# Optimization experiments

Hardware: AMD Instinct MI355X
Metric: run time of the kernel (lower is better)

## Reference

```python
import jax, jax.numpy as jnp
import numpy as np

N_OBJ = 20000
N_TRI = 100000
D = 512      # input_dim_obj == input_dim_pred == output_dim
H = 512      # hidden_dim


def _kaiming(key, fan_out, fan_in):
    return jax.random.normal(key, (fan_out, fan_in), jnp.float32) * jnp.sqrt(2.0 / fan_in)


def setup_inputs() -> dict:
    key = jax.random.key(0)
    ks = jax.random.split(key, 12)
    obj_vecs = jax.random.normal(ks[0], (N_OBJ, D), jnp.float32)
    pred_vecs = jax.random.normal(ks[1], (N_TRI, D), jnp.float32)
    edges = jax.random.randint(ks[2], (N_TRI, 2), 0, N_OBJ, jnp.int32)
    Din1 = 2 * D + D            # net1 input: 1536
    Dout1 = 2 * H + D           # net1 output: 1536
    return {
        "obj_vecs": obj_vecs,
        "pred_vecs": pred_vecs,
        "edges": edges,
        "W1": _kaiming(ks[3], H, Din1), "b1": jnp.zeros((H,), jnp.float32),
        "W2": _kaiming(ks[4], Dout1, H), "b2": jnp.zeros((Dout1,), jnp.float32),
        "V1": _kaiming(ks[5], H, H), "c1": jnp.zeros((H,), jnp.float32),
        "V2": _kaiming(ks[6], D, H), "c2": jnp.zeros((D,), jnp.float32),
        "P_obj": jax.random.normal(ks[7], (D, D), jnp.float32) * (1.0 / jnp.sqrt(D)),
        "pb_obj": jnp.zeros((D,), jnp.float32),
        "P_pred": jax.random.normal(ks[8], (D, D), jnp.float32) * (1.0 / jnp.sqrt(D)),
        "pb_pred": jnp.zeros((D,), jnp.float32),
    }


def reference(obj_vecs, pred_vecs, edges, W1, b1, W2, b2, V1, c1, V2, c2,
              P_obj, pb_obj, P_pred, pb_pred):
    num_objs = obj_vecs.shape[0]
    s_idx = edges[:, 0]
    o_idx = edges[:, 1]
    # gather + concat: [T, 2*D + D]
    cur_t = jnp.concatenate([obj_vecs[s_idx], pred_vecs, obj_vecs[o_idx]], axis=1)
    # net1: Linear -> ReLU -> Linear -> ReLU (final_nonlinearity=True)
    h = jax.nn.relu(cur_t @ W1.T + b1)
    new_t = jax.nn.relu(h @ W2.T + b2)            # [T, 2H + D]
    new_s = new_t[:, :H]
    new_p = new_t[:, H:H + D]
    new_o = new_t[:, H + D:2 * H + D]
    # scatter_add pooling
    pooled = jax.ops.segment_sum(new_s, s_idx, num_segments=num_objs)
    pooled = pooled + jax.ops.segment_sum(new_o, o_idx, num_segments=num_objs)
    # avg pooling normalization
    ones = jnp.ones((edges.shape[0],), jnp.float32)
    counts = jax.ops.segment_sum(ones, s_idx, num_segments=num_objs)
    counts = counts + jax.ops.segment_sum(ones, o_idx, num_segments=num_objs)
    counts = jnp.maximum(counts, 1.0)
    pooled = pooled / counts[:, None]
    # net2: Linear -> ReLU -> Linear -> ReLU
    g = jax.nn.relu(pooled @ V1.T + c1)
    new_obj = jax.nn.relu(g @ V2.T + c2)
    # residual projections
    new_obj = new_obj + obj_vecs @ P_obj.T + pb_obj
    new_p = new_p + pred_vecs @ P_pred.T + pb_pred
    return new_obj, new_p
```

## Files before the change

kernel.cpp:

```cpp
#include <hip/hip_runtime.h>
#include <stdint.h>

#define NOBJ 20000
#define NTRI 100000

typedef unsigned short ushort_t;
typedef __attribute__((ext_vector_type(8))) short short8;
typedef __attribute__((ext_vector_type(4))) float float4v;

enum { MODE_H = 0, MODE_G = 2, MODE_OBJ = 3, MODE_PRED = 4, MODE_SO = 5, MODE_P = 6 };

__device__ __forceinline__ ushort_t f2bf(float f) {
    union { float f; unsigned int i; } x;
    x.f = f;
    unsigned int r = x.i + 0x7fffu + ((x.i >> 16) & 1u);
    return (ushort_t)(r >> 16);
}

__device__ __forceinline__ void gload_lds16(const ushort_t* g, short8* l) {
    __builtin_amdgcn_global_load_lds((const __attribute__((address_space(1))) void*)g,
                                     (__attribute__((address_space(3))) void*)l,
                                     16, 0, 0);
}

__global__ void __launch_bounds__(256) cvt_k(const float* __restrict__ src,
                                             ushort_t* __restrict__ dst, int n4) {
    int i = blockIdx.x * 256 + threadIdx.x;
    if (i >= n4) return;
    const float4* s4 = (const float4*)src;
    float4 v = s4[i];
    ushort_t o[4] = {f2bf(v.x), f2bf(v.y), f2bf(v.z), f2bf(v.w)};
    *(uint64_t*)(dst + 4 * (size_t)i) = *(const uint64_t*)o;
}

__global__ void __launch_bounds__(256) hist_k(const int* __restrict__ edges,
                                              int* __restrict__ counts_s,
                                              int* __restrict__ counts_o, int n2) {
    int i = blockIdx.x * 256 + threadIdx.x;
    if (i >= n2) return;
    int obj = edges[i];
    if (i & 1) atomicAdd(&counts_o[obj], 1);
    else       atomicAdd(&counts_s[obj], 1);
}

__global__ void __launch_bounds__(256) scan_k(const int* __restrict__ counts,
                                              int* __restrict__ offs,
                                              int* __restrict__ cur, int n) {
    __shared__ int lds[256];
    const int CHUNK = 80;
    int t = threadIdx.x;
    int base = t * CHUNK;
    int s = 0;
    for (int j = 0; j < CHUNK; ++j) {
        int i = base + j;
        if (i < n) s += counts[i];
    }
    lds[t] = s;
    __syncthreads();
    for (int off = 1; off < 256; off <<= 1) {
        int v = (t >= off) ? lds[t - off] : 0;
        __syncthreads();
        lds[t] += v;
        __syncthreads();
    }
    int run = lds[t] - s;
    for (int j = 0; j < CHUNK; ++j) {
        int i = base + j;
        if (i < n) {
            offs[i] = run;
            cur[i] = run;
            run += counts[i];
        } else if (i == n) {
            offs[n] = run;
        }
    }
}

__global__ void __launch_bounds__(256) fill_k(const int* __restrict__ edges,
                                              int* __restrict__ cur_s, int* __restrict__ cur_o,
                                              int* __restrict__ perm_s, int* __restrict__ perm_o,
                                              int n) {
    int t = blockIdx.x * 256 + threadIdx.x;
    if (t >= n) return;
    int s = edges[2 * t];
    int o = edges[2 * t + 1];
    perm_s[atomicAdd(&cur_s[s], 1)] = t;
    perm_o[atomicAdd(&cur_o[o], 1)] = t;
}

template <int PASS>
__global__ void __launch_bounds__(256)
pool_k(const ushort_t* __restrict__ nst, const int* __restrict__ offs_s,
       const int* __restrict__ offs_o, float* __restrict__ pooled) {
    int wave = threadIdx.x >> 6;
    int lane = threadIdx.x & 63;
    int obj = blockIdx.x * 4 + wave;
    if (obj >= NOBJ) return;
    const int* offs = (PASS == 0) ? offs_s : offs_o;
    int s = offs[obj], e = offs[obj + 1];
    float acc[8];
#pragma unroll
    for (int j = 0; j < 8; ++j) acc[j] = 0.f;
    for (int i = s; i < e; ++i) {
        uint4 v = *(const uint4*)(nst + (size_t)i * 512 + lane * 8);
        acc[0] += __uint_as_float(v.x << 16);
        acc[1] += __uint_as_float(v.x & 0xffff0000u);
        acc[2] += __uint_as_float(v.y << 16);
        acc[3] += __uint_as_float(v.y & 0xffff0000u);
        acc[4] += __uint_as_float(v.z << 16);
        acc[5] += __uint_as_float(v.z & 0xffff0000u);
        acc[6] += __uint_as_float(v.w << 16);
        acc[7] += __uint_as_float(v.w & 0xffff0000u);
    }
    float* prow = pooled + (size_t)obj * 512 + lane * 8;
    if (PASS == 0) {
        *(float4*)(prow)     = make_float4(acc[0], acc[1], acc[2], acc[3]);
        *(float4*)(prow + 4) = make_float4(acc[4], acc[5], acc[6], acc[7]);
    } else {
        float4 a0 = *(const float4*)(prow);
        float4 a1 = *(const float4*)(prow + 4);
        int deg = (offs_s[obj + 1] - offs_s[obj]) + (offs_o[obj + 1] - offs_o[obj]);
        float inv = 1.f / (float)((deg > 1) ? deg : 1);
        *(float4*)(prow)     = make_float4((acc[0] + a0.x) * inv, (acc[1] + a0.y) * inv,
                                           (acc[2] + a0.z) * inv, (acc[3] + a0.w) * inv);
        *(float4*)(prow + 4) = make_float4((acc[4] + a1.x) * inv, (acc[5] + a1.y) * inv,
                                           (acc[6] + a1.z) * inv, (acc[7] + a1.w) * inv);
    }
}

template <int MODE>
__global__ void __launch_bounds__(256)
gtc_gemm(const ushort_t* __restrict__ A, const ushort_t* __restrict__ Bw,
         const float* __restrict__ bias,
         const ushort_t* __restrict__ A2, const ushort_t* __restrict__ B2,
         const float* __restrict__ bias2,
         const int* __restrict__ idx,
         const ushort_t* __restrict__ objv, const ushort_t* __restrict__ predv,
         const float* __restrict__ addend,
         void* __restrict__ outv,
         int M, int K, int lda)
{
    __shared__ short8 sA[1024];
    __shared__ short8 sB[1024];
    __shared__ int sIdx[128];
    __shared__ int oIdx[128];

    const int tid  = threadIdx.x;
    const int lane = tid & 63;
    const int wave = tid >> 6;
    const int wm   = wave & 1;
    const int wn   = wave >> 1;
    const int quad = lane >> 4;
    const int lr   = lane & 15;
    const int m0   = blockIdx.y * 128;
    const int n0   = blockIdx.x * 128;

    if (MODE == MODE_H) {
        if (tid < 128) {
            int t = m0 + tid;
            if (t >= M) t = M - 1;
            sIdx[tid] = idx[2 * t];
            oIdx[tid] = idx[2 * t + 1];
        }
        __syncthreads();
    } else if (MODE == MODE_SO) {
        if (tid < 128) {
            int t = m0 + tid;
            if (t >= M) t = M - 1;
            sIdx[tid] = idx[t];
        }
        __syncthreads();
    }

    float4v acc[4][4];
#pragma unroll
    for (int i = 0; i < 4; ++i)
#pragma unroll
        for (int j = 0; j < 4; ++j)
            acc[i][j] = (float4v){0.f, 0.f, 0.f, 0.f};

    const int npass = (MODE == MODE_OBJ) ? 2 : 1;
    for (int pass = 0; pass < npass; ++pass) {
        const ushort_t* Ap = (pass == 0) ? A : A2;
        const ushort_t* Bp = (pass == 0) ? Bw : B2;

        for (int k0 = 0; k0 < K; k0 += 64) {
            __syncthreads();
#pragma unroll
            for (int i = 0; i < 4; ++i) {
                int g  = i * 256 + tid;
                int kg = g >> 7;
                int m  = g & 127;
                int krow = k0 + kg * 8;
                const ushort_t* src;
                if (MODE == MODE_H) {
                    int t = m0 + m;
                    if (t >= M) t = M - 1;
                    if (krow < 512)
                        src = objv + (size_t)sIdx[m] * 512 + krow;
                    else if (krow < 1024)
                        src = predv + (size_t)t * 512 + (krow - 512);
                    else
                        src = objv + (size_t)oIdx[m] * 512 + (krow - 1024);
                } else if (MODE == MODE_SO) {
                    src = Ap + (size_t)sIdx[m] * (size_t)K + krow;
                } else {
                    int r = m0 + m;
                    if (r >= M) r = M - 1;
                    src = Ap + (size_t)r * (size_t)lda + krow;
                }
                gload_lds16(src, &sA[g]);
            }
#pragma unroll
            for (int i = 0; i < 4; ++i) {
                int g  = i * 256 + tid;
                int kg = g >> 7;
                int n  = g & 127;
                gload_lds16(Bp + (size_t)(n0 + n) * K + k0 + kg * 8, &sB[g]);
            }
            __syncthreads();

#pragma unroll
            for (int kk = 0; kk < 2; ++kk) {
                short8 af[4], bfv[4];
#pragma unroll
                for (int t = 0; t < 4; ++t)
                    af[t] = sA[(kk * 4 + quad) * 128 + wm * 64 + t * 16 + lr];
#pragma unroll
                for (int t = 0; t < 4; ++t)
                    bfv[t] = sB[(kk * 4 + quad) * 128 + wn * 64 + t * 16 + lr];
#pragma unroll
                for (int ti = 0; ti < 4; ++ti)
#pragma unroll
                    for (int tj = 0; tj < 4; ++tj)
                        acc[ti][tj] = __builtin_amdgcn_mfma_f32_16x16x32_bf16(
                            af[ti], bfv[tj], acc[ti][tj], 0, 0, 0);
            }
        }

        if (MODE == MODE_OBJ && pass == 0) {
#pragma unroll
            for (int tj = 0; tj < 4; ++tj) {
                float b = bias[n0 + wn * 64 + tj * 16 + lr];
#pragma unroll
                for (int ti = 0; ti < 4; ++ti)
#pragma unroll
                    for (int r = 0; r < 4; ++r)
                        acc[ti][tj][r] = fmaxf(acc[ti][tj][r] + b, 0.f);
            }
        }
    }

    float bcol[4];
#pragma unroll
    for (int tj = 0; tj < 4; ++tj) {
        int col = n0 + wn * 64 + tj * 16 + lr;
        const float* bptr = (MODE == MODE_OBJ) ? bias2 : bias;
        bcol[tj] = bptr[col];
    }

#pragma unroll
    for (int ti = 0; ti < 4; ++ti) {
#pragma unroll
        for (int r = 0; r < 4; ++r) {
            int row = m0 + wm * 64 + ti * 16 + quad * 4 + r;
            if (row >= M) continue;
#pragma unroll
            for (int tj = 0; tj < 4; ++tj) {
                int col = n0 + wn * 64 + tj * 16 + lr;
                float v = acc[ti][tj][r];
                if (MODE == MODE_H || MODE == MODE_G || MODE == MODE_SO) {
                    v = fmaxf(v + bcol[tj], 0.f);
                    ((ushort_t*)outv)[(size_t)row * 512 + col] = f2bf(v);
                } else if (MODE == MODE_P) {
                    v = fmaxf(v + bcol[tj], 0.f) + addend[(size_t)row * 512 + col];
                    ((float*)outv)[(size_t)row * 512 + col] = v;
                } else if (MODE == MODE_OBJ) {
                    ((float*)outv)[(size_t)row * 512 + col] = v + bcol[tj];
                } else {
                    v = v + bcol[tj];
                    if (addend) v += addend[(size_t)row * 512 + col];
                    ((float*)outv)[(size_t)row * 512 + col] = v;
                }
            }
        }
    }
}

extern "C" void kernel_launch(void* const* d_in, const int* in_sizes, int n_in,
                              void* d_out, int out_size, void* d_ws, size_t ws_size,
                              hipStream_t stream) {
    const float* obj    = (const float*)d_in[0];
    const float* pred   = (const float*)d_in[1];
    const int*   edges  = (const int*)d_in[2];
    const float* W1     = (const float*)d_in[3];
    const float* b1     = (const float*)d_in[4];
    const float* W2     = (const float*)d_in[5];
    const float* b2     = (const float*)d_in[6];
    const float* V1     = (const float*)d_in[7];
    const float* c1     = (const float*)d_in[8];
    const float* V2     = (const float*)d_in[9];
    const float* c2     = (const float*)d_in[10];
    const float* Pobj   = (const float*)d_in[11];
    const float* pbobj  = (const float*)d_in[12];
    const float* Ppred  = (const float*)d_in[13];
    const float* pbpred = (const float*)d_in[14];

    char* ws = (char*)d_ws;
    ushort_t* h       = (ushort_t*)(ws + 0);
    ushort_t* bfPred  = (ushort_t*)(ws + 102400000);
    ushort_t* nst     = bfPred;
    ushort_t* bfObj   = (ushort_t*)(ws + 204800000);
    ushort_t* bfW1    = (ushort_t*)(ws + 225280000);
    char* csr = ws + 225280000;
    int* counts_s = (int*)(csr + 0);
    int* counts_o = (int*)(csr + 80000);
    int* offs_s   = (int*)(csr + 160000);
    int* offs_o   = (int*)(csr + 240064);
    int* cur_s    = (int*)(csr + 320128);
    int* cur_o    = (int*)(csr + 400128);
    int* perm_s   = (int*)(csr + 480128);
    int* perm_o   = (int*)(csr + 880128);
    ushort_t* bfW2    = (ushort_t*)(ws + 226852864);
    ushort_t* bfV1    = (ushort_t*)(ws + 228425728);
    ushort_t* bfV2    = (ushort_t*)(ws + 228950016);
    ushort_t* bfPobj  = (ushort_t*)(ws + 229474304);
    ushort_t* bfPpred = (ushort_t*)(ws + 229998592);
    ushort_t* pooledn = (ushort_t*)(ws + 0);
    ushort_t* gbuf    = (ushort_t*)(ws + 20480000);

    float* out_obj = (float*)d_out;
    float* out_p   = out_obj + (size_t)NOBJ * 512;
    float* pooled = out_obj;

    cvt_k<<<dim3(10000), dim3(256), 0, stream>>>(obj,   bfObj,   10240000 / 4);
    cvt_k<<<dim3(50000), dim3(256), 0, stream>>>(pred,  bfPred,  51200000 / 4);
    cvt_k<<<dim3(768),   dim3(256), 0, stream>>>(W1,    bfW1,    786432 / 4);
    cvt_k<<<dim3(768),   dim3(256), 0, stream>>>(W2,    bfW2,    786432 / 4);
    cvt_k<<<dim3(256),   dim3(256), 0, stream>>>(V1,    bfV1,    262144 / 4);
    cvt_k<<<dim3(256),   dim3(256), 0, stream>>>(V2,    bfV2,    262144 / 4);
    cvt_k<<<dim3(256),   dim3(256), 0, stream>>>(Pobj,  bfPobj,  262144 / 4);
    cvt_k<<<dim3(256),   dim3(256), 0, stream>>>(Ppred, bfPpred, 262144 / 4);

    gtc_gemm<MODE_PRED><<<dim3(4, 782), dim3(256), 0, stream>>>(
        bfPred, bfPpred, pbpred, nullptr, nullptr, nullptr,
        nullptr, nullptr, nullptr, nullptr, out_p, NTRI, 512, 512);

    gtc_gemm<MODE_H><<<dim3(4, 782), dim3(256), 0, stream>>>(
        nullptr, bfW1, b1, nullptr, nullptr, nullptr,
        edges, bfObj, bfPred, nullptr, h, NTRI, 1536, 1536);

    hipMemsetAsync(counts_s, 0, 160000, stream);
    hist_k<<<dim3(782), dim3(256), 0, stream>>>(edges, counts_s, counts_o, 2 * NTRI);
    scan_k<<<dim3(1), dim3(256), 0, stream>>>(counts_s, offs_s, cur_s, NOBJ);
    scan_k<<<dim3(1), dim3(256), 0, stream>>>(counts_o, offs_o, cur_o, NOBJ);
    fill_k<<<dim3(391), dim3(256), 0, stream>>>(edges, cur_s, cur_o, perm_s, perm_o, NTRI);

    gtc_gemm<MODE_SO><<<dim3(4, 782), dim3(256), 0, stream>>>(
        h, bfW2, b2, nullptr, nullptr, nullptr,
        perm_s, nullptr, nullptr, nullptr, nst, NTRI, 512, 512);
    pool_k<0><<<dim3(5000), dim3(256), 0, stream>>>(nst, offs_s, offs_o, pooled);

    gtc_gemm<MODE_SO><<<dim3(4, 782), dim3(256), 0, stream>>>(
        h, bfW2 + 1024 * 512, b2 + 1024, nullptr, nullptr, nullptr,
        perm_o, nullptr, nullptr, nullptr, nst, NTRI, 512, 512);
    pool_k<1><<<dim3(5000), dim3(256), 0, stream>>>(nst, offs_s, offs_o, pooled);

    gtc_gemm<MODE_P><<<dim3(4, 782), dim3(256), 0, stream>>>(
        h, bfW2 + 512 * 512, b2 + 512, nullptr, nullptr, nullptr,
        nullptr, nullptr, nullptr, out_p, out_p, NTRI, 512, 512);

    cvt_k<<<dim3(10000), dim3(256), 0, stream>>>(pooled, pooledn, 10240000 / 4);

    gtc_gemm<MODE_G><<<dim3(4, 157), dim3(256), 0, stream>>>(
        pooledn, bfV1, c1, nullptr, nullptr, nullptr,
        nullptr, nullptr, nullptr, nullptr, gbuf, NOBJ, 512, 512);

    gtc_gemm<MODE_OBJ><<<dim3(4, 157), dim3(256), 0, stream>>>(
        gbuf, bfV2, c2, bfObj, bfPobj, pbobj,
        nullptr, nullptr, nullptr, nullptr, out_obj, NOBJ, 512, 512);
}
```

Baseline: 1.714 ms.

## Fuse pred residual projection into new_p GEMM and remap blocks across XCDs

The separate pred@P_pred GEMM and the later new_p GEMM are replaced by one two-pass MODE_OBJ launch. It accumulates relu(h@W2p+b2p) and then pred@P_pred into the same accumulators, so out_p is written once in fp32 instead of being written, re-read and rewritten. Work-group indices are remapped so consecutive tiles land on the same XCD, which should improve L2 reuse of the shared B and A rows. Per-thread gather base pointers are also hoisted out of the K loop. The MODE_PRED and MODE_P paths and the addend parameter are removed.

After: 1.591 ms. 1.08x faster.

```diff
diff --git a/kernel.cpp b/kernel.cpp
--- a/kernel.cpp
+++ b/kernel.cpp
@@ -8,7 +8,7 @@
 typedef __attribute__((ext_vector_type(8))) short short8;
 typedef __attribute__((ext_vector_type(4))) float float4v;
 
-enum { MODE_H = 0, MODE_G = 2, MODE_OBJ = 3, MODE_PRED = 4, MODE_SO = 5, MODE_P = 6 };
+enum { MODE_H = 0, MODE_G = 2, MODE_OBJ = 3, MODE_SO = 5 };
 
 __device__ __forceinline__ ushort_t f2bf(float f) {
     union { float f; unsigned int i; } x;
@@ -136,7 +136,6 @@
          const float* __restrict__ bias2,
          const int* __restrict__ idx,
          const ushort_t* __restrict__ objv, const ushort_t* __restrict__ predv,
-         const float* __restrict__ addend,
          void* __restrict__ outv,
          int M, int K, int lda)
 {
@@ -152,8 +151,17 @@
     const int wn   = wave >> 1;
     const int quad = lane >> 4;
     const int lr   = lane & 15;
-    const int m0   = blockIdx.y * 128;
-    const int n0   = blockIdx.x * 128;
+
+    const int nx  = gridDim.x;
+    const int nwg = nx * gridDim.y;
+    {
+    }
+    const int lb   = blockIdx.y * nx + blockIdx.x;
+    const int q    = nwg >> 3, r = nwg & 7;
+    const int xcd  = lb & 7, slot = lb >> 3;
+    const int w    = xcd * q + ((xcd < r) ? xcd : r) + slot;
+    const int m0   = (w / nx) * 128;
+    const int n0   = (w % nx) * 128;
 
     if (MODE == MODE_H) {
         if (tid < 128) {
@@ -172,6 +180,31 @@
         __syncthreads();
     }
 
+    int mI[4], kgI[4];
+#pragma unroll
+    for (int i = 0; i < 4; ++i) {
+        int g = i * 256 + tid;
+        kgI[i] = g >> 7;
+        mI[i]  = g & 127;
+    }
+
+    const ushort_t *bA0[4], *bA1[4], *bA2[4];
+    if (MODE == MODE_H) {
+#pragma unroll
+        for (int i = 0; i < 4; ++i) {
+            int m = mI[i];
+            int t = m0 + m;
+            if (t >= M) t = M - 1;
+            bA0[i] = objv + (size_t)sIdx[m] * 512;
+            bA1[i] = predv + (size_t)t * 512 - 512;
+            bA2[i] = objv + (size_t)oIdx[m] * 512 - 1024;
+        }
+    } else if (MODE == MODE_SO) {
+#pragma unroll
+        for (int i = 0; i < 4; ++i)
+            bA0[i] = A + (size_t)sIdx[mI[i]] * (size_t)K;
+    }
+
     float4v acc[4][4];
 #pragma unroll
     for (int i = 0; i < 4; ++i)
@@ -184,40 +217,36 @@
         const ushort_t* Ap = (pass == 0) ? A : A2;
         const ushort_t* Bp = (pass == 0) ? Bw : B2;
 
+        const ushort_t *pA[4], *pB[4];
+#pragma unroll
+        for (int i = 0; i < 4; ++i) {
+            if (MODE == MODE_SO) {
+                pA[i] = bA0[i];
+            } else if (MODE != MODE_H) {
+                int rr = m0 + mI[i];
+                if (rr >= M) rr = M - 1;
+                pA[i] = Ap + (size_t)rr * (size_t)lda;
+            }
+            pB[i] = Bp + (size_t)(n0 + mI[i]) * (size_t)K;
+        }
+
         for (int k0 = 0; k0 < K; k0 += 64) {
             __syncthreads();
 #pragma unroll
             for (int i = 0; i < 4; ++i) {
-                int g  = i * 256 + tid;
-                int kg = g >> 7;
-                int m  = g & 127;
-                int krow = k0 + kg * 8;
+                int krow = k0 + kgI[i] * 8;
                 const ushort_t* src;
-                if (MODE == MODE_H) {
-                    int t = m0 + m;
-                    if (t >= M) t = M - 1;
-                    if (krow < 512)
-                        src = objv + (size_t)sIdx[m] * 512 + krow;
-                    else if (krow < 1024)
-                        src = predv + (size_t)t * 512 + (krow - 512);
-                    else
-                        src = objv + (size_t)oIdx[m] * 512 + (krow - 1024);
-                } else if (MODE == MODE_SO) {
-                    src = Ap + (size_t)sIdx[m] * (size_t)K + krow;
-                } else {
-                    int r = m0 + m;
-                    if (r >= M) r = M - 1;
-                    src = Ap + (size_t)r * (size_t)lda + krow;
-                }
-                gload_lds16(src, &sA[g]);
+                if (MODE == MODE_H)
+                    src = (krow < 512)  ? bA0[i] + krow
+                        : (krow < 1024) ? bA1[i] + krow
+                        :                 bA2[i] + krow;
+                else
+                    src = pA[i] + krow;
+                gload_lds16(src, &sA[i * 256 + tid]);
             }
 #pragma unroll
-            for (int i = 0; i < 4; ++i) {
-                int g  = i * 256 + tid;
-                int kg = g >> 7;
-                int n  = g & 127;
-                gload_lds16(Bp + (size_t)(n0 + n) * K + k0 + kg * 8, &sB[g]);
-            }
+            for (int i = 0; i < 4; ++i)
+                gload_lds16(pB[i] + k0 + kgI[i] * 8, &sB[i * 256 + tid]);
             __syncthreads();
 
 #pragma unroll
@@ -269,18 +298,11 @@
             for (int tj = 0; tj < 4; ++tj) {
                 int col = n0 + wn * 64 + tj * 16 + lr;
                 float v = acc[ti][tj][r];
-                if (MODE == MODE_H || MODE == MODE_G || MODE == MODE_SO) {
+                if (MODE == MODE_OBJ) {
+                    ((float*)outv)[(size_t)row * 512 + col] = v + bcol[tj];
+                } else {
                     v = fmaxf(v + bcol[tj], 0.f);
                     ((ushort_t*)outv)[(size_t)row * 512 + col] = f2bf(v);
-                } else if (MODE == MODE_P) {
-                    v = fmaxf(v + bcol[tj], 0.f) + addend[(size_t)row * 512 + col];
-                    ((float*)outv)[(size_t)row * 512 + col] = v;
-                } else if (MODE == MODE_OBJ) {
-                    ((float*)outv)[(size_t)row * 512 + col] = v + bcol[tj];
-                } else {
-                    v = v + bcol[tj];
-                    if (addend) v += addend[(size_t)row * 512 + col];
-                    ((float*)outv)[(size_t)row * 512 + col] = v;
                 }
             }
         }
@@ -342,13 +364,9 @@
     cvt_k<<<dim3(256),   dim3(256), 0, stream>>>(Pobj,  bfPobj,  262144 / 4);
     cvt_k<<<dim3(256),   dim3(256), 0, stream>>>(Ppred, bfPpred, 262144 / 4);
 
-    gtc_gemm<MODE_PRED><<<dim3(4, 782), dim3(256), 0, stream>>>(
-        bfPred, bfPpred, pbpred, nullptr, nullptr, nullptr,
-        nullptr, nullptr, nullptr, nullptr, out_p, NTRI, 512, 512);
-
     gtc_gemm<MODE_H><<<dim3(4, 782), dim3(256), 0, stream>>>(
         nullptr, bfW1, b1, nullptr, nullptr, nullptr,
-        edges, bfObj, bfPred, nullptr, h, NTRI, 1536, 1536);
+        edges, bfObj, bfPred, h, NTRI, 1536, 1536);
 
     hipMemsetAsync(counts_s, 0, 160000, stream);
     hist_k<<<dim3(782), dim3(256), 0, stream>>>(edges, counts_s, counts_o, 2 * NTRI);
@@ -356,27 +374,27 @@
     scan_k<<<dim3(1), dim3(256), 0, stream>>>(counts_o, offs_o, cur_o, NOBJ);
     fill_k<<<dim3(391), dim3(256), 0, stream>>>(edges, cur_s, cur_o, perm_s, perm_o, NTRI);
 
+    gtc_gemm<MODE_OBJ><<<dim3(4, 782), dim3(256), 0, stream>>>(
+        h, bfW2 + 512 * 512, b2 + 512, bfPred, bfPpred, pbpred,
+        nullptr, nullptr, nullptr, out_p, NTRI, 512, 512);
+
     gtc_gemm<MODE_SO><<<dim3(4, 782), dim3(256), 0, stream>>>(
         h, bfW2, b2, nullptr, nullptr, nullptr,
-        perm_s, nullptr, nullptr, nullptr, nst, NTRI, 512, 512);
+        perm_s, nullptr, nullptr, nst, NTRI, 512, 512);
     pool_k<0><<<dim3(5000), dim3(256), 0, stream>>>(nst, offs_s, offs_o, pooled);
 
     gtc_gemm<MODE_SO><<<dim3(4, 782), dim3(256), 0, stream>>>(
         h, bfW2 + 1024 * 512, b2 + 1024, nullptr, nullptr, nullptr,
-        perm_o, nullptr, nullptr, nullptr, nst, NTRI, 512, 512);
+        perm_o, nullptr, nullptr, nst, NTRI, 512, 512);
     pool_k<1><<<dim3(5000), dim3(256), 0, stream>>>(nst, offs_s, offs_o, pooled);
-
-    gtc_gemm<MODE_P><<<dim3(4, 782), dim3(256), 0, stream>>>(
-        h, bfW2 + 512 * 512, b2 + 512, nullptr, nullptr, nullptr,
-        nullptr, nullptr, nullptr, out_p, out_p, NTRI, 512, 512);
 
     cvt_k<<<dim3(10000), dim3(256), 0, stream>>>(pooled, pooledn, 10240000 / 4);
 
     gtc_gemm<MODE_G><<<dim3(4, 157), dim3(256), 0, stream>>>(
         pooledn, bfV1, c1, nullptr, nullptr, nullptr,
-        nullptr, nullptr, nullptr, nullptr, gbuf, NOBJ, 512, 512);
+        nullptr, nullptr, nullptr, gbuf, NOBJ, 512, 512);
 
     gtc_gemm<MODE_OBJ><<<dim3(4, 157), dim3(256), 0, stream>>>(
         gbuf, bfV2, c2, bfObj, bfPobj, pbobj,
-        nullptr, nullptr, nullptr, nullptr, out_obj, NOBJ, 512, 512);
-}
+        nullptr, nullptr, nullptr, out_obj, NOBJ, 512, 512);
+}
```
